# Kernel optimization log

Measured on AMD Instinct MI355X. Metric: run time of the kernel, lower is better.

## Reference

```python
import jax, jax.numpy as jnp
import numpy as np

NUM_ITERS = 10
G_KSIZE, G_SIGMA = 5, 0.5
BIL_KSIZE, BIL_SIG_COLOR, BIL_SIG_SPACE = 5, 0.5, 5.0
EDGE_KSIZE, EDGE_SIG_COLOR, EDGE_SIG_SPACE = 5, 0.5, 5.0


def _gauss1d(ksize, sigma):
    x = jnp.arange(ksize, dtype=jnp.float32) - ksize // 2  # odd ksize -> centered (kornia)
    g = jnp.exp(-(x * x) / (2.0 * sigma * sigma))
    return g / g.sum()


def gaussian_blur(q, ksize, sigma):
    # separable gaussian blur with reflect padding, kornia GaussianBlur2d semantics
    k = _gauss1d(ksize, sigma)
    r = ksize // 2
    B, C, H, W = q.shape
    qp = jnp.pad(q, ((0, 0), (0, 0), (r, r), (0, 0)), mode='reflect')
    q = sum(k[i] * qp[:, :, i:i + H, :] for i in range(ksize))
    qp = jnp.pad(q, ((0, 0), (0, 0), (0, 0), (r, r)), mode='reflect')
    q = sum(k[i] * qp[:, :, :, i:i + W] for i in range(ksize))
    return q


def bilateral_weights(guide, ksize, sigma_color, sigma_space):
    # kornia joint_bilateral_blur weights (l1 color distance, reflect border).
    # guide: [B, Cg, H, W] -> weights [B, K*K, H, W]; guidance is constant across
    # CRF iterations so we precompute the kernel once.
    B, Cg, H, W = guide.shape
    r = ksize // 2
    g1 = _gauss1d(ksize, sigma_space)
    space = jnp.outer(g1, g1)  # normalized 2d gaussian (kornia get_gaussian_kernel2d)
    gp = jnp.pad(guide, ((0, 0), (0, 0), (r, r), (r, r)), mode='reflect')
    inv2sc2 = -0.5 / (sigma_color * sigma_color)
    ws = []
    for dy in range(ksize):
        for dx in range(ksize):
            d = jnp.abs(gp[:, :, dy:dy + H, dx:dx + W] - guide).sum(axis=1)  # [B,H,W]
            ws.append(space[dy, dx] * jnp.exp(inv2sc2 * d * d))
    return jnp.stack(ws, axis=1)  # [B, K*K, H, W]


def bilateral_apply(q, weights, ksize):
    # q: [B,C,H,W], weights: [B,K*K,H,W]
    B, C, H, W = q.shape
    r = ksize // 2
    qp = jnp.pad(q, ((0, 0), (0, 0), (r, r), (r, r)), mode='reflect')
    num = jnp.zeros_like(q)
    idx = 0
    for dy in range(ksize):
        for dx in range(ksize):
            num = num + weights[:, idx][:, None] * qp[:, :, dy:dy + H, dx:dx + W]
            idx += 1
    den = weights.sum(axis=1)[:, None]  # [B,1,H,W]
    return num / den


def _compat(f):
    # compat matrix is -1 off-diagonal, 0 on diagonal:
    # pairwise[c] = -sum_{c'!=c} f[c'] = f[c] - sum_{c'} f[c']
    return f - f.sum(axis=1, keepdims=True)


def setup_inputs() -> dict:
    key = jax.random.key(0)
    k1, k2, k3 = jax.random.split(key, 3)
    B, C, H, W = 2, 21, 512, 512
    unary_logits = jax.random.normal(k1, (B, C, H, W), dtype=jnp.float32)
    image = jax.random.uniform(k2, (B, 3, H, W), dtype=jnp.float32)
    edges = jax.random.uniform(k3, (B, H, W), dtype=jnp.float32)
    return {"unary_logits": unary_logits, "image": image, "edges": edges}


def reference(unary_logits, image, edges):
    edges4 = edges[:, None]  # [B,1,H,W]
    w_rgb = bilateral_weights(image, BIL_KSIZE, BIL_SIG_COLOR, BIL_SIG_SPACE)
    w_edge = bilateral_weights(edges4, EDGE_KSIZE, EDGE_SIG_COLOR, EDGE_SIG_SPACE)
    q = jax.nn.softmax(unary_logits, axis=1)
    for _ in range(NUM_ITERS):
        sf = gaussian_blur(q, G_KSIZE, G_SIGMA)
        rf = bilateral_apply(q, w_rgb, BIL_KSIZE)
        ef = bilateral_apply(q, w_edge, EDGE_KSIZE)
        pairwise = _compat(sf) + _compat(rf) + _compat(ef)
        q = jax.nn.softmax(unary_logits - pairwise, axis=1)
    return q
```

## Files before the change

kernel.cpp:

```cpp
#include <hip/hip_runtime.h>
#include <math.h>

#define BATCH 2
#define NCH 21
#define CPAD 24
#define HH 512
#define WW 512
#define KS 5
#define RAD 2
#define NTAPS 25
#define NUM_ITERS 10

#define TXW 32
#define TYW 8
#define HXW (TXW + 2*RAD)
#define HYW (TYW + 2*RAD)
#define HPXW (HXW * HYW)

#define TW 32
#define TH 16
#define NTHR 512
#define SX 40
#define SY 24
#define SPX (SX * SY)
#define SCHUNK (SPX * 3)
#define EX 36
#define EY 20
#define EPX (EX * EY)
#define RING (EPX - TW*TH)

typedef _Float16 f16;
typedef _Float16 half8 __attribute__((ext_vector_type(8)));
typedef _Float16 half2v __attribute__((ext_vector_type(2)));

__device__ __forceinline__ int refl(int i, int n) {
    if (i < 0) i = -i;
    if (i >= n) i = 2*n - 2 - i;
    return i;
}

#define WSEL(h0, h1, h2, hl, t) \
    ((t) < 8 ? (h0)[(t)] : (t) < 16 ? (h1)[(t) - 8] : (t) < 24 ? (h2)[(t) - 16] : (hl))

__global__ __launch_bounds__(256) void weights_kernel(const float* __restrict__ image,
                                                      const float* __restrict__ edges,
                                                      f16* __restrict__ wcA,
                                                      f16* __restrict__ wcB16) {
    __shared__ float sr_[HYW][HXW];
    __shared__ float sg_[HYW][HXW];
    __shared__ float sb_[HYW][HXW];
    __shared__ float se_[HYW][HXW];

    const int tx = threadIdx.x;
    const int ty = threadIdx.y;
    const int tid = ty * TXW + tx;
    const int x0 = blockIdx.x * TXW;
    const int y0 = blockIdx.y * TYW;
    const int b = blockIdx.z;
    const int x = x0 + tx;
    const int y = y0 + ty;
    const size_t plane = (size_t)HH * WW;
    const float* img = image + (size_t)b * 3 * plane;
    const float* edg = edges + (size_t)b * plane;

    for (int i = tid; i < HPXW; i += TXW * TYW) {
        int ly = i / HXW, lx = i - ly * HXW;
        int gy = refl(y0 + ly - RAD, HH);
        int gx = refl(x0 + lx - RAD, WW);
        int g = gy * WW + gx;
        sr_[ly][lx] = img[g];
        sg_[ly][lx] = img[plane + g];
        sb_[ly][lx] = img[2 * plane + g];
        se_[ly][lx] = edg[g];
    }
    __syncthreads();

    float gs[3];
    gs[0] = 1.0f; gs[1] = __expf(-1.0f / 50.0f); gs[2] = __expf(-4.0f / 50.0f);
    float gb[3];
    gb[0] = 1.0f; gb[1] = __expf(-2.0f); gb[2] = __expf(-8.0f);
    float gbs = gb[0] + 2.0f * (gb[1] + gb[2]);
    gb[0] /= gbs; gb[1] /= gbs; gb[2] /= gbs;

    const float r0 = sr_[ty + RAD][tx + RAD];
    const float g0 = sg_[ty + RAD][tx + RAD];
    const float b0 = sb_[ty + RAD][tx + RAD];
    const float e0 = se_[ty + RAD][tx + RAD];

    float wr[NTAPS], we[NTAPS];
    float sr = 0.f, se = 0.f;
#pragma unroll
    for (int dy = 0; dy < KS; dy++) {
#pragma unroll
        for (int dx = 0; dx < KS; dx++) {
            float sp = gs[abs(dy - RAD)] * gs[abs(dx - RAD)];
            float d = fabsf(sr_[ty + dy][tx + dx] - r0)
                    + fabsf(sg_[ty + dy][tx + dx] - g0)
                    + fabsf(sb_[ty + dy][tx + dx] - b0);
            float w1 = sp * __expf(-2.0f * d * d);
            float de = fabsf(se_[ty + dy][tx + dx] - e0);
            float w2 = sp * __expf(-2.0f * de * de);
            wr[dy * KS + dx] = w1;
            we[dy * KS + dx] = w2;
            sr += w1;
            se += w2;
        }
    }
    float isr = 1.0f / sr, ise = 1.0f / se;
    float wt[NTAPS];
#pragma unroll
    for (int t = 0; t < NTAPS; t++) {
        int dy = t / KS, dx = t % KS;
        float g2 = gb[abs(dy - RAD)] * gb[abs(dx - RAD)];
        wt[t] = g2 + wr[t] * isr + we[t] * ise;
    }
    const size_t pixoff = (size_t)b * plane + (size_t)y * WW + x;
    half8* wo = (half8*)(wcA + pixoff * 24);
#pragma unroll
    for (int g = 0; g < 3; g++) {
        half8 v;
#pragma unroll
        for (int k = 0; k < 8; k++) v[k] = (f16)wt[g * 8 + k];
        wo[g] = v;
    }
    wcB16[pixoff] = (f16)wt[24];
}

__global__ void init_kernel(const float* __restrict__ unary,
                            f16* __restrict__ q,
                            f16* __restrict__ u16) {
    int idx = blockIdx.x * blockDim.x + threadIdx.x;
    if (idx >= BATCH * HH * WW) return;
    int p = idx % (HH * WW);
    int b = idx / (HH * WW);
    const size_t plane = (size_t)HH * WW;
    const float* u = unary + (size_t)b * NCH * plane + p;
    float l[CPAD];
    float m = -1e30f;
#pragma unroll
    for (int c = 0; c < NCH; c++) { l[c] = u[c * plane]; m = fmaxf(m, l[c]); }
    l[21] = 0.f; l[22] = 0.f; l[23] = 0.f;

    half8* uo = (half8*)(u16 + ((size_t)b * plane + p) * CPAD);
#pragma unroll
    for (int g = 0; g < 3; g++) {
        half8 v;
#pragma unroll
        for (int k = 0; k < 8; k++) v[k] = (f16)l[g * 8 + k];
        uo[g] = v;
    }

    float s = 0.f;
    float e[CPAD];
#pragma unroll
    for (int c = 0; c < NCH; c++) { e[c] = __expf(l[c] - m); s += e[c]; }
    float is = 1.0f / s;
    e[21] = 0.f; e[22] = 0.f; e[23] = 0.f;
    half8* qo = (half8*)(q + ((size_t)b * plane + p) * CPAD);
#pragma unroll
    for (int g = 0; g < 3; g++) {
        half8 v;
#pragma unroll
        for (int k = 0; k < 8; k++) v[k] = (f16)(e[g * 8 + k] * is);
        qo[g] = v;
    }
}

#define CONV_ACC_PK(acc2, lds, row0, col0, stride, W0, W1, W2, WL)                     \
    {                                                                                  \
        _Pragma("unroll")                                                              \
        for (int dy = 0; dy < KS; dy++) {                                              \
            _Pragma("unroll")                                                          \
            for (int dx = 0; dx < KS; dx++) {                                          \
                const f16 wt_ = WSEL(W0, W1, W2, WL, dy * KS + dx);                    \
                const half2v wv_ = {wt_, wt_};                                         \
                const f16* tp = (lds) + ((size_t)((row0) + dy) * (stride) + (col0) + dx) * CPAD; \
                half8 v0 = *(const half8*)(tp);                                        \
                half8 v1 = *(const half8*)(tp + 8);                                    \
                half8 v2 = *(const half8*)(tp + 16);                                   \
                acc2[0]  = __builtin_elementwise_fma(wv_, __builtin_shufflevector(v0, v0, 0, 1), acc2[0]);  \
                acc2[1]  = __builtin_elementwise_fma(wv_, __builtin_shufflevector(v0, v0, 2, 3), acc2[1]);  \
                acc2[2]  = __builtin_elementwise_fma(wv_, __builtin_shufflevector(v0, v0, 4, 5), acc2[2]);  \
                acc2[3]  = __builtin_elementwise_fma(wv_, __builtin_shufflevector(v0, v0, 6, 7), acc2[3]);  \
                acc2[4]  = __builtin_elementwise_fma(wv_, __builtin_shufflevector(v1, v1, 0, 1), acc2[4]);  \
                acc2[5]  = __builtin_elementwise_fma(wv_, __builtin_shufflevector(v1, v1, 2, 3), acc2[5]);  \
                acc2[6]  = __builtin_elementwise_fma(wv_, __builtin_shufflevector(v1, v1, 4, 5), acc2[6]);  \
                acc2[7]  = __builtin_elementwise_fma(wv_, __builtin_shufflevector(v1, v1, 6, 7), acc2[7]);  \
                acc2[8]  = __builtin_elementwise_fma(wv_, __builtin_shufflevector(v2, v2, 0, 1), acc2[8]);  \
                acc2[9]  = __builtin_elementwise_fma(wv_, __builtin_shufflevector(v2, v2, 2, 3), acc2[9]);  \
                acc2[10] = __builtin_elementwise_fma(wv_, __builtin_shufflevector(v2, v2, 4, 5), acc2[10]); \
            }                                                                          \
        }                                                                              \
    }

#define LOGITS_FROM_PK(l, acc2, U0, U1, U2)                                            \
    {                                                                                  \
        _Pragma("unroll")                                                              \
        for (int j = 0; j < 10; j++) {                                                 \
            l[2 * j]     = -(float)acc2[j][0];                                         \
            l[2 * j + 1] = -(float)acc2[j][1];                                         \
        }                                                                              \
        l[20] = -(float)acc2[10][0];                                                   \
        _Pragma("unroll")                                                              \
        for (int k = 0; k < 8; k++) l[k] += (float)U0[k];                              \
        _Pragma("unroll")                                                              \
        for (int k = 0; k < 8; k++) l[8 + k] += (float)U1[k];                          \
        _Pragma("unroll")                                                              \
        for (int k = 0; k < 5; k++) l[16 + k] += (float)U2[k];                         \
    }

template <bool FINAL>
__global__ __launch_bounds__(NTHR, 4) void crf_pair_kernel(const f16* __restrict__ qin,
                                                           const f16* __restrict__ u16,
                                                           const f16* __restrict__ wcA,
                                                           const f16* __restrict__ wcB16,
                                                           void* __restrict__ qout) {
    __shared__ __align__(16) f16 buf[SPX][CPAD];

    const int tid = threadIdx.x;
    const int ix = tid & (TW - 1);
    const int iy = tid >> 5;

    const int flat = blockIdx.x;
    const int band = flat & 7;
    const int within = flat >> 3;
    const int b = within >> 6;
    const int r = within & 63;
    const int x0 = (r & 15) * TW;
    const int y0 = (band * 4 + (r >> 4)) * TH;
    const int gx = x0 + ix;
    const int gy = y0 + iy;
    const size_t plane = (size_t)HH * WW;

    const f16* qbase = qin + (size_t)b * plane * CPAD;
    f16* lbase = &buf[0][0];
    for (int idx = tid; idx < SCHUNK; idx += NTHR) {
        int px = idx / 3, h4 = idx - px * 3;
        int sly = px / SX, slx = px - sly * SX;
        int qy = refl(y0 - 4 + sly, HH);
        int qx = refl(x0 - 4 + slx, WW);
        const f16* g = qbase + ((size_t)(qy * WW + qx)) * CPAD + h4 * 8;
        __builtin_amdgcn_global_load_lds(
            (const __attribute__((address_space(1))) void*)g,
            (__attribute__((address_space(3))) void*)(lbase + (size_t)idx * 8),
            16, 0, 0);
    }

    const size_t pixoff = (size_t)b * plane + (size_t)gy * WW + gx;
    const half8* wp = (const half8*)(wcA + pixoff * 24);
    half8 wa0 = wp[0], wa1 = wp[1], wa2 = wp[2];
    f16 wl = wcB16[pixoff];
    const half8* up = (const half8*)(u16 + pixoff * CPAD);
    half8 ui0 = up[0], ui1 = up[1], ui2 = up[2];

    const bool has_ring = tid < RING;
    int rly = 0, rlx = 0;
    half8 wr0 = {}, wr1 = {}, wr2 = {}, ur0 = {}, ur1 = {}, ur2 = {};
    f16 wrl = (f16)0.f;
    if (has_ring) {
        int t = tid;
        if (t < 72)       { rly = t / 36;       rlx = t % 36; }
        else if (t < 144) { t -= 72;  rly = 18 + t / 36; rlx = t % 36; }
        else              { t -= 144; rly = 2 + (t >> 2); int c = t & 3; rlx = (c < 2) ? c : (c + 32); }
        int rgy = y0 + rly - 2, rgx = x0 + rlx - 2;
        int cy = min(max(rgy, 0), HH - 1);
        int cx = min(max(rgx, 0), WW - 1);
        size_t rpo = (size_t)b * plane + (size_t)cy * WW + cx;
        const half8* wpr = (const half8*)(wcA + rpo * 24);
        wr0 = wpr[0]; wr1 = wpr[1]; wr2 = wpr[2];
        wrl = wcB16[rpo];
        const half8* upr = (const half8*)(u16 + rpo * CPAD);
        ur0 = upr[0]; ur1 = upr[1]; ur2 = upr[2];
    }

    __syncthreads();

    half8 qr0, qr1, qr2;
    if (has_ring) {
        half2v acc2[11];
#pragma unroll
        for (int j = 0; j < 11; j++) acc2[j] = (half2v){(f16)0.f, (f16)0.f};
        CONV_ACC_PK(acc2, lbase, rly, rlx, SX, wr0, wr1, wr2, wrl);
        float l[NCH];
        LOGITS_FROM_PK(l, acc2, ur0, ur1, ur2);
        float m = l[0];
#pragma unroll
        for (int c = 1; c < NCH; c++) m = fmaxf(m, l[c]);
        float s = 0.f;
#pragma unroll
        for (int c = 0; c < NCH; c++) { l[c] = __expf(l[c] - m); s += l[c]; }
        float is = 1.0f / s;
#pragma unroll
        for (int k = 0; k < 8; k++) qr0[k] = (f16)(l[k] * is);
#pragma unroll
        for (int k = 0; k < 8; k++) qr1[k] = (f16)(l[8 + k] * is);
#pragma unroll
        for (int k = 0; k < 5; k++) qr2[k] = (f16)(l[16 + k] * is);
        qr2[5] = (f16)0.f; qr2[6] = (f16)0.f; qr2[7] = (f16)0.f;
    }

    half8 qi0, qi1, qi2;
    {
        half2v acc2[11];
#pragma unroll
        for (int j = 0; j < 11; j++) acc2[j] = (half2v){(f16)0.f, (f16)0.f};
        CONV_ACC_PK(acc2, lbase, iy + 2, ix + 2, SX, wa0, wa1, wa2, wl);
        float l[NCH];
        LOGITS_FROM_PK(l, acc2, ui0, ui1, ui2);
        float m = l[0];
#pragma unroll
        for (int c = 1; c < NCH; c++) m = fmaxf(m, l[c]);
        float s = 0.f;
#pragma unroll
        for (int c = 0; c < NCH; c++) { l[c] = __expf(l[c] - m); s += l[c]; }
        float is = 1.0f / s;
#pragma unroll
        for (int k = 0; k < 8; k++) qi0[k] = (f16)(l[k] * is);
#pragma unroll
        for (int k = 0; k < 8; k++) qi1[k] = (f16)(l[8 + k] * is);
#pragma unroll
        for (int k = 0; k < 5; k++) qi2[k] = (f16)(l[16 + k] * is);
        qi2[5] = (f16)0.f; qi2[6] = (f16)0.f; qi2[7] = (f16)0.f;
    }

    __syncthreads();

    {
        half8* d = (half8*)(lbase + ((size_t)(iy + 2) * EX + (ix + 2)) * CPAD);
        d[0] = qi0; d[1] = qi1; d[2] = qi2;
        if (has_ring) {
            half8* dr = (half8*)(lbase + ((size_t)rly * EX + rlx) * CPAD);
            dr[0] = qr0; dr[1] = qr1; dr[2] = qr2;
        }
    }

    __syncthreads();

    {
        int ry[KS], rx[KS];
#pragma unroll
        for (int d = 0; d < KS; d++) {
            ry[d] = refl(gy + d - 2, HH) - (y0 - 2);
            rx[d] = refl(gx + d - 2, WW) - (x0 - 2);
        }
        half2v acc2[11];
#pragma unroll
        for (int j = 0; j < 11; j++) acc2[j] = (half2v){(f16)0.f, (f16)0.f};
#pragma unroll
        for (int dy = 0; dy < KS; dy++) {
#pragma unroll
            for (int dx = 0; dx < KS; dx++) {
                const f16 wt_ = WSEL(wa0, wa1, wa2, wl, dy * KS + dx);
                const half2v wv_ = {wt_, wt_};
                const f16* tp = lbase + ((size_t)ry[dy] * EX + rx[dx]) * CPAD;
                half8 v0 = *(const half8*)(tp);
                half8 v1 = *(const half8*)(tp + 8);
                half8 v2 = *(const half8*)(tp + 16);
                acc2[0]  = __builtin_elementwise_fma(wv_, __builtin_shufflevector(v0, v0, 0, 1), acc2[0]);
                acc2[1]  = __builtin_elementwise_fma(wv_, __builtin_shufflevector(v0, v0, 2, 3), acc2[1]);
                acc2[2]  = __builtin_elementwise_fma(wv_, __builtin_shufflevector(v0, v0, 4, 5), acc2[2]);
                acc2[3]  = __builtin_elementwise_fma(wv_, __builtin_shufflevector(v0, v0, 6, 7), acc2[3]);
                acc2[4]  = __builtin_elementwise_fma(wv_, __builtin_shufflevector(v1, v1, 0, 1), acc2[4]);
                acc2[5]  = __builtin_elementwise_fma(wv_, __builtin_shufflevector(v1, v1, 2, 3), acc2[5]);
                acc2[6]  = __builtin_elementwise_fma(wv_, __builtin_shufflevector(v1, v1, 4, 5), acc2[6]);
                acc2[7]  = __builtin_elementwise_fma(wv_, __builtin_shufflevector(v1, v1, 6, 7), acc2[7]);
                acc2[8]  = __builtin_elementwise_fma(wv_, __builtin_shufflevector(v2, v2, 0, 1), acc2[8]);
                acc2[9]  = __builtin_elementwise_fma(wv_, __builtin_shufflevector(v2, v2, 2, 3), acc2[9]);
                acc2[10] = __builtin_elementwise_fma(wv_, __builtin_shufflevector(v2, v2, 4, 5), acc2[10]);
            }
        }
        float l[NCH];
        LOGITS_FROM_PK(l, acc2, ui0, ui1, ui2);
        float m = l[0];
#pragma unroll
        for (int c = 1; c < NCH; c++) m = fmaxf(m, l[c]);
        float s = 0.f;
#pragma unroll
        for (int c = 0; c < NCH; c++) { l[c] = __expf(l[c] - m); s += l[c]; }
        float is = 1.0f / s;

        if (FINAL) {
            float* qo = (float*)qout + (size_t)b * NCH * plane + (size_t)gy * WW + gx;
#pragma unroll
            for (int c = 0; c < NCH; c++) qo[c * plane] = l[c] * is;
        } else {
            half8* qo = (half8*)((f16*)qout + pixoff * CPAD);
            half8 o0, o1, o2;
#pragma unroll
            for (int k = 0; k < 8; k++) o0[k] = (f16)(l[k] * is);
#pragma unroll
            for (int k = 0; k < 8; k++) o1[k] = (f16)(l[8 + k] * is);
#pragma unroll
            for (int k = 0; k < 5; k++) o2[k] = (f16)(l[16 + k] * is);
            o2[5] = (f16)0.f; o2[6] = (f16)0.f; o2[7] = (f16)0.f;
            qo[0] = o0; qo[1] = o1; qo[2] = o2;
        }
    }
}

extern "C" void kernel_launch(void* const* d_in, const int* in_sizes, int n_in,
                              void* d_out, int out_size, void* d_ws, size_t ws_size,
                              hipStream_t stream) {
    const float* unary = (const float*)d_in[0];
    const float* image = (const float*)d_in[1];
    const float* edges = (const float*)d_in[2];
    float* out = (float*)d_out;

    const size_t plane = (size_t)HH * WW;
    char* ws = (char*)d_ws;
    f16* wcA = (f16*)ws;
    char* p1 = ws + sizeof(f16) * BATCH * plane * 24;
    f16* wcB16 = (f16*)p1;
    char* p2 = p1 + sizeof(f16) * BATCH * plane;
    f16* u16 = (f16*)p2;
    char* p3 = p2 + sizeof(f16) * BATCH * plane * CPAD;
    f16* qA = (f16*)p3;
    f16* qB = qA + (size_t)BATCH * plane * CPAD;

    const int npix = BATCH * HH * WW;
    dim3 gridW(WW / TXW, HH / TYW, BATCH);
    dim3 blockW(TXW, TYW, 1);
    weights_kernel<<<gridW, blockW, 0, stream>>>(image, edges, wcA, wcB16);
    init_kernel<<<(npix + 255) / 256, 256, 0, stream>>>(unary, qA, u16);

    const int nblk = (WW / TW) * (HH / TH) * BATCH;
    f16* qa = qA;
    f16* qb = qB;
    const int npairs = NUM_ITERS / 2;
    for (int it = 0; it < npairs - 1; it++) {
        crf_pair_kernel<false><<<nblk, NTHR, 0, stream>>>(qa, u16, wcA, wcB16, (void*)qb);
        f16* t = qa; qa = qb; qb = t;
    }
    crf_pair_kernel<true><<<nblk, NTHR, 0, stream>>>(qa, u16, wcA, wcB16, (void*)out);
}
```

Measured before the change: 287.5 us.

## Compute two vertical pixels per thread and double tile height

The CRF pair kernel tile height doubles from 16 to 32 rows, with the LDS staging region and the recomputed halo ring resized to match. Each thread now computes two vertically adjacent pixels and sweeps six LDS rows instead of two separate five-row windows, so each LDS load feeds both pixels. This shrinks the halo recompute overhead relative to tile area and cuts LDS reads per output. In exchange it roughly doubles accumulator and weight register use and raises LDS per block, which may reduce occupancy or cause spills under the existing launch bounds.

```diff
diff --git a/kernel.cpp b/kernel.cpp
--- a/kernel.cpp
+++ b/kernel.cpp
@@ -18,14 +18,14 @@
 #define HPXW (HXW * HYW)
 
 #define TW 32
-#define TH 16
+#define TH 32
 #define NTHR 512
 #define SX 40
-#define SY 24
+#define SY 40
 #define SPX (SX * SY)
 #define SCHUNK (SPX * 3)
 #define EX 36
-#define EY 20
+#define EY 36
 #define EPX (EX * EY)
 #define RING (EPX - TW*TH)
 
@@ -166,6 +166,21 @@
     }
 }
 
+#define TAP_PK(acc2, v0, v1, v2, wv_)                                                           \
+    {                                                                                           \
+        acc2[0]  = __builtin_elementwise_fma(wv_, __builtin_shufflevector(v0, v0, 0, 1), acc2[0]);  \
+        acc2[1]  = __builtin_elementwise_fma(wv_, __builtin_shufflevector(v0, v0, 2, 3), acc2[1]);  \
+        acc2[2]  = __builtin_elementwise_fma(wv_, __builtin_shufflevector(v0, v0, 4, 5), acc2[2]);  \
+        acc2[3]  = __builtin_elementwise_fma(wv_, __builtin_shufflevector(v0, v0, 6, 7), acc2[3]);  \
+        acc2[4]  = __builtin_elementwise_fma(wv_, __builtin_shufflevector(v1, v1, 0, 1), acc2[4]);  \
+        acc2[5]  = __builtin_elementwise_fma(wv_, __builtin_shufflevector(v1, v1, 2, 3), acc2[5]);  \
+        acc2[6]  = __builtin_elementwise_fma(wv_, __builtin_shufflevector(v1, v1, 4, 5), acc2[6]);  \
+        acc2[7]  = __builtin_elementwise_fma(wv_, __builtin_shufflevector(v1, v1, 6, 7), acc2[7]);  \
+        acc2[8]  = __builtin_elementwise_fma(wv_, __builtin_shufflevector(v2, v2, 0, 1), acc2[8]);  \
+        acc2[9]  = __builtin_elementwise_fma(wv_, __builtin_shufflevector(v2, v2, 2, 3), acc2[9]);  \
+        acc2[10] = __builtin_elementwise_fma(wv_, __builtin_shufflevector(v2, v2, 4, 5), acc2[10]); \
+    }
+
 #define CONV_ACC_PK(acc2, lds, row0, col0, stride, W0, W1, W2, WL)                     \
     {                                                                                  \
         _Pragma("unroll")                                                              \
@@ -178,17 +193,7 @@
                 half8 v0 = *(const half8*)(tp);                                        \
                 half8 v1 = *(const half8*)(tp + 8);                                    \
                 half8 v2 = *(const half8*)(tp + 16);                                   \
-                acc2[0]  = __builtin_elementwise_fma(wv_, __builtin_shufflevector(v0, v0, 0, 1), acc2[0]);  \
-                acc2[1]  = __builtin_elementwise_fma(wv_, __builtin_shufflevector(v0, v0, 2, 3), acc2[1]);  \
-                acc2[2]  = __builtin_elementwise_fma(wv_, __builtin_shufflevector(v0, v0, 4, 5), acc2[2]);  \
-                acc2[3]  = __builtin_elementwise_fma(wv_, __builtin_shufflevector(v0, v0, 6, 7), acc2[3]);  \
-                acc2[4]  = __builtin_elementwise_fma(wv_, __builtin_shufflevector(v1, v1, 0, 1), acc2[4]);  \
-                acc2[5]  = __builtin_elementwise_fma(wv_, __builtin_shufflevector(v1, v1, 2, 3), acc2[5]);  \
-                acc2[6]  = __builtin_elementwise_fma(wv_, __builtin_shufflevector(v1, v1, 4, 5), acc2[6]);  \
-                acc2[7]  = __builtin_elementwise_fma(wv_, __builtin_shufflevector(v1, v1, 6, 7), acc2[7]);  \
-                acc2[8]  = __builtin_elementwise_fma(wv_, __builtin_shufflevector(v2, v2, 0, 1), acc2[8]);  \
-                acc2[9]  = __builtin_elementwise_fma(wv_, __builtin_shufflevector(v2, v2, 2, 3), acc2[9]);  \
-                acc2[10] = __builtin_elementwise_fma(wv_, __builtin_shufflevector(v2, v2, 4, 5), acc2[10]); \
+                TAP_PK(acc2, v0, v1, v2, wv_);                                         \
             }                                                                          \
         }                                                                              \
     }
@@ -207,6 +212,24 @@
         for (int k = 0; k < 8; k++) l[8 + k] += (float)U1[k];                          \
         _Pragma("unroll")                                                              \
         for (int k = 0; k < 5; k++) l[16 + k] += (float)U2[k];                         \
+    }
+
+#define SOFTMAX_PACK(l, O0, O1, O2)                                                    \
+    {                                                                                  \
+        float m = l[0];                                                                \
+        _Pragma("unroll")                                                              \
+        for (int c = 1; c < NCH; c++) m = fmaxf(m, l[c]);                              \
+        float s = 0.f;                                                                 \
+        _Pragma("unroll")                                                              \
+        for (int c = 0; c < NCH; c++) { l[c] = __expf(l[c] - m); s += l[c]; }          \
+        float is = 1.0f / s;                                                           \
+        _Pragma("unroll")                                                              \
+        for (int k = 0; k < 8; k++) O0[k] = (f16)(l[k] * is);                          \
+        _Pragma("unroll")                                                              \
+        for (int k = 0; k < 8; k++) O1[k] = (f16)(l[8 + k] * is);                      \
+        _Pragma("unroll")                                                              \
+        for (int k = 0; k < 5; k++) O2[k] = (f16)(l[16 + k] * is);                     \
+        O2[5] = (f16)0.f; O2[6] = (f16)0.f; O2[7] = (f16)0.f;                          \
     }
 
 template <bool FINAL>
@@ -218,18 +241,18 @@
     __shared__ __align__(16) f16 buf[SPX][CPAD];
 
     const int tid = threadIdx.x;
-    const int ix = tid & (TW - 1);
-    const int iy = tid >> 5;
+    const int ixv = tid & (TW - 1);
+    const int iyv = tid >> 5;
 
     const int flat = blockIdx.x;
     const int band = flat & 7;
     const int within = flat >> 3;
-    const int b = within >> 6;
-    const int r = within & 63;
+    const int b = within >> 5;
+    const int r = within & 31;
     const int x0 = (r & 15) * TW;
-    const int y0 = (band * 4 + (r >> 4)) * TH;
-    const int gx = x0 + ix;
-    const int gy = y0 + iy;
+    const int y0 = (band * 2 + (r >> 4)) * TH;
+    const int gx = x0 + ixv;
+    const int gy0 = y0 + 2 * iyv;
     const size_t plane = (size_t)HH * WW;
 
     const f16* qbase = qin + (size_t)b * plane * CPAD;
@@ -246,12 +269,18 @@
             16, 0, 0);
     }
 
-    const size_t pixoff = (size_t)b * plane + (size_t)gy * WW + gx;
-    const half8* wp = (const half8*)(wcA + pixoff * 24);
-    half8 wa0 = wp[0], wa1 = wp[1], wa2 = wp[2];
-    f16 wl = wcB16[pixoff];
-    const half8* up = (const half8*)(u16 + pixoff * CPAD);
-    half8 ui0 = up[0], ui1 = up[1], ui2 = up[2];
+    const size_t pixoff0 = (size_t)b * plane + (size_t)gy0 * WW + gx;
+    const size_t pixoff1 = pixoff0 + WW;
+    const half8* wp0 = (const half8*)(wcA + pixoff0 * 24);
+    half8 wa0 = wp0[0], wa1 = wp0[1], wa2 = wp0[2];
+    f16 wl0 = wcB16[pixoff0];
+    const half8* wp1 = (const half8*)(wcA + pixoff1 * 24);
+    half8 wb0 = wp1[0], wb1 = wp1[1], wb2 = wp1[2];
+    f16 wl1 = wcB16[pixoff1];
+    const half8* up0 = (const half8*)(u16 + pixoff0 * CPAD);
+    half8 uA0 = up0[0], uA1 = up0[1], uA2 = up0[2];
+    const half8* up1 = (const half8*)(u16 + pixoff1 * CPAD);
+    half8 uB0 = up1[0], uB1 = up1[1], uB2 = up1[2];
 
     const bool has_ring = tid < RING;
     int rly = 0, rlx = 0;
@@ -259,9 +288,8 @@
     f16 wrl = (f16)0.f;
     if (has_ring) {
         int t = tid;
-        if (t < 72)       { rly = t / 36;       rlx = t % 36; }
-        else if (t < 144) { t -= 72;  rly = 18 + t / 36; rlx = t % 36; }
-        else              { t -= 144; rly = 2 + (t >> 2); int c = t & 3; rlx = (c < 2) ? c : (c + 32); }
+        if (t < 144) { int rr = t / 36; rly = (rr < 2) ? rr : 32 + rr; rlx = t % 36; }
+        else         { int t2 = t - 144; rly = 2 + (t2 >> 2); int c = t2 & 3; rlx = (c < 2) ? c : (c + 32); }
         int rgy = y0 + rly - 2, rgx = x0 + rlx - 2;
         int cy = min(max(rgy, 0), HH - 1);
         int cx = min(max(rgx, 0), WW - 1);
@@ -283,51 +311,53 @@
         CONV_ACC_PK(acc2, lbase, rly, rlx, SX, wr0, wr1, wr2, wrl);
         float l[NCH];
         LOGITS_FROM_PK(l, acc2, ur0, ur1, ur2);
-        float m = l[0];
-#pragma unroll
-        for (int c = 1; c < NCH; c++) m = fmaxf(m, l[c]);
-        float s = 0.f;
-#pragma unroll
-        for (int c = 0; c < NCH; c++) { l[c] = __expf(l[c] - m); s += l[c]; }
-        float is = 1.0f / s;
-#pragma unroll
-        for (int k = 0; k < 8; k++) qr0[k] = (f16)(l[k] * is);
-#pragma unroll
-        for (int k = 0; k < 8; k++) qr1[k] = (f16)(l[8 + k] * is);
-#pragma unroll
-        for (int k = 0; k < 5; k++) qr2[k] = (f16)(l[16 + k] * is);
-        qr2[5] = (f16)0.f; qr2[6] = (f16)0.f; qr2[7] = (f16)0.f;
-    }
-
-    half8 qi0, qi1, qi2;
+        SOFTMAX_PACK(l, qr0, qr1, qr2);
+    }
+
+    half8 qiA0, qiA1, qiA2, qiB0, qiB1, qiB2;
     {
-        half2v acc2[11];
-#pragma unroll
-        for (int j = 0; j < 11; j++) acc2[j] = (half2v){(f16)0.f, (f16)0.f};
-        CONV_ACC_PK(acc2, lbase, iy + 2, ix + 2, SX, wa0, wa1, wa2, wl);
+        half2v accA[11], accB[11];
+#pragma unroll
+        for (int j = 0; j < 11; j++) {
+            accA[j] = (half2v){(f16)0.f, (f16)0.f};
+            accB[j] = (half2v){(f16)0.f, (f16)0.f};
+        }
+        const int row0 = 2 * iyv + 2;
+        const int col0 = ixv + 2;
+#pragma unroll
+        for (int dy = 0; dy < 6; dy++) {
+#pragma unroll
+            for (int dx = 0; dx < KS; dx++) {
+                const f16* tp = lbase + ((size_t)(row0 + dy) * SX + col0 + dx) * CPAD;
+                half8 v0 = *(const half8*)(tp);
+                half8 v1 = *(const half8*)(tp + 8);
+                half8 v2 = *(const half8*)(tp + 16);
+                if (dy < 5) {
+                    const f16 wt_ = WSEL(wa0, wa1, wa2, wl0, dy * KS + dx);
+                    const half2v wv_ = {wt_, wt_};
+                    TAP_PK(accA, v0, v1, v2, wv_);
+                }
+                if (dy >= 1) {
+                    const f16 wt_ = WSEL(wb0, wb1, wb2, wl1, (dy - 1) * KS + dx);
+                    const half2v wv_ = {wt_, wt_};
+                    TAP_PK(accB, v0, v1, v2, wv_);
+                }
+            }
+        }
         float l[NCH];
-        LOGITS_FROM_PK(l, acc2, ui0, ui1, ui2);
-        float m = l[0];
-#pragma unroll
-        for (int c = 1; c < NCH; c++) m = fmaxf(m, l[c]);
-        float s = 0.f;
-#pragma unroll
-        for (int c = 0; c < NCH; c++) { l[c] = __expf(l[c] - m); s += l[c]; }
-        float is = 1.0f / s;
-#pragma unroll
-        for (int k = 0; k < 8; k++) qi0[k] = (f16)(l[k] * is);
-#pragma unroll
-        for (int k = 0; k < 8; k++) qi1[k] = (f16)(l[8 + k] * is);
-#pragma unroll
-        for (int k = 0; k < 5; k++) qi2[k] = (f16)(l[16 + k] * is);
-        qi2[5] = (f16)0.f; qi2[6] = (f16)0.f; qi2[7] = (f16)0.f;
+        LOGITS_FROM_PK(l, accA, uA0, uA1, uA2);
+        SOFTMAX_PACK(l, qiA0, qiA1, qiA2);
+        LOGITS_FROM_PK(l, accB, uB0, uB1, uB2);
+        SOFTMAX_PACK(l, qiB0, qiB1, qiB2);
     }
 
     __syncthreads();
 
     {
-        half8* d = (half8*)(lbase + ((size_t)(iy + 2) * EX + (ix + 2)) * CPAD);
-        d[0] = qi0; d[1] = qi1; d[2] = qi2;
+        half8* d0 = (half8*)(lbase + ((size_t)(2 * iyv + 2) * EX + (ixv + 2)) * CPAD);
+        d0[0] = qiA0; d0[1] = qiA1; d0[2] = qiA2;
+        half8* d1 = (half8*)(lbase + ((size_t)(2 * iyv + 3) * EX + (ixv + 2)) * CPAD);
+        d1[0] = qiB0; d1[1] = qiB1; d1[2] = qiB2;
         if (has_ring) {
             half8* dr = (half8*)(lbase + ((size_t)rly * EX + rlx) * CPAD);
             dr[0] = qr0; dr[1] = qr1; dr[2] = qr2;
@@ -337,63 +367,67 @@
     __syncthreads();
 
     {
-        int ry[KS], rx[KS];
-#pragma unroll
-        for (int d = 0; d < KS; d++) {
-            ry[d] = refl(gy + d - 2, HH) - (y0 - 2);
-            rx[d] = refl(gx + d - 2, WW) - (x0 - 2);
-        }
-        half2v acc2[11];
-#pragma unroll
-        for (int j = 0; j < 11; j++) acc2[j] = (half2v){(f16)0.f, (f16)0.f};
-#pragma unroll
-        for (int dy = 0; dy < KS; dy++) {
+        int ryy[6], rxx[KS];
+#pragma unroll
+        for (int d = 0; d < 6; d++) ryy[d] = refl(gy0 + d - 2, HH) - (y0 - 2);
+#pragma unroll
+        for (int d = 0; d < KS; d++) rxx[d] = refl(gx + d - 2, WW) - (x0 - 2);
+
+        half2v accA[11], accB[11];
+#pragma unroll
+        for (int j = 0; j < 11; j++) {
+            accA[j] = (half2v){(f16)0.f, (f16)0.f};
+            accB[j] = (half2v){(f16)0.f, (f16)0.f};
+        }
+#pragma unroll
+        for (int dy = 0; dy < 6; dy++) {
 #pragma unroll
             for (int dx = 0; dx < KS; dx++) {
-                const f16 wt_ = WSEL(wa0, wa1, wa2, wl, dy * KS + dx);
-                const half2v wv_ = {wt_, wt_};
-                const f16* tp = lbase + ((size_t)ry[dy] * EX + rx[dx]) * CPAD;
+                const f16* tp = lbase + ((size_t)ryy[dy] * EX + rxx[dx]) * CPAD;
                 half8 v0 = *(const half8*)(tp);
                 half8 v1 = *(const half8*)(tp + 8);
                 half8 v2 = *(const half8*)(tp + 16);
-                acc2[0]  = __builtin_elementwise_fma(wv_, __builtin_shufflevector(v0, v0, 0, 1), acc2[0]);
-                acc2[1]  = __builtin_elementwise_fma(wv_, __builtin_shufflevector(v0, v0, 2, 3), acc2[1]);
-                acc2[2]  = __builtin_elementwise_fma(wv_, __builtin_shufflevector(v0, v0, 4, 5), acc2[2]);
-                acc2[3]  = __builtin_elementwise_fma(wv_, __builtin_shufflevector(v0, v0, 6, 7), acc2[3]);
-                acc2[4]  = __builtin_elementwise_fma(wv_, __builtin_shufflevector(v1, v1, 0, 1), acc2[4]);
-                acc2[5]  = __builtin_elementwise_fma(wv_, __builtin_shufflevector(v1, v1, 2, 3), acc2[5]);
-                acc2[6]  = __builtin_elementwise_fma(wv_, __builtin_shufflevector(v1, v1, 4, 5), acc2[6]);
-                acc2[7]  = __builtin_elementwise_fma(wv_, __builtin_shufflevector(v1, v1, 6, 7), acc2[7]);
-                acc2[8]  = __builtin_elementwise_fma(wv_, __builtin_shufflevector(v2, v2, 0, 1), acc2[8]);
-                acc2[9]  = __builtin_elementwise_fma(wv_, __builtin_shufflevector(v2, v2, 2, 3), acc2[9]);
-                acc2[10] = __builtin_elementwise_fma(wv_, __builtin_shufflevector(v2, v2, 4, 5), acc2[10]);
+                if (dy < 5) {
+                    const f16 wt_ = WSEL(wa0, wa1, wa2, wl0, dy * KS + dx);
+                    const half2v wv_ = {wt_, wt_};
+                    TAP_PK(accA, v0, v1, v2, wv_);
+                }
+                if (dy >= 1) {
+                    const f16 wt_ = WSEL(wb0, wb1, wb2, wl1, (dy - 1) * KS + dx);
+                    const half2v wv_ = {wt_, wt_};
+                    TAP_PK(accB, v0, v1, v2, wv_);
+                }
             }
         }
-        float l[NCH];
-        LOGITS_FROM_PK(l, acc2, ui0, ui1, ui2);
-        float m = l[0];
-#pragma unroll
-        for (int c = 1; c < NCH; c++) m = fmaxf(m, l[c]);
-        float s = 0.f;
-#pragma unroll
-        for (int c = 0; c < NCH; c++) { l[c] = __expf(l[c] - m); s += l[c]; }
-        float is = 1.0f / s;
+        float l0[NCH], l1[NCH];
+        LOGITS_FROM_PK(l0, accA, uA0, uA1, uA2);
+        LOGITS_FROM_PK(l1, accB, uB0, uB1, uB2);
 
         if (FINAL) {
-            float* qo = (float*)qout + (size_t)b * NCH * plane + (size_t)gy * WW + gx;
-#pragma unroll
-            for (int c = 0; c < NCH; c++) qo[c * plane] = l[c] * is;
+            float m0 = l0[0], m1 = l1[0];
+#pragma unroll
+            for (int c = 1; c < NCH; c++) { m0 = fmaxf(m0, l0[c]); m1 = fmaxf(m1, l1[c]); }
+            float s0 = 0.f, s1 = 0.f;
+#pragma unroll
+            for (int c = 0; c < NCH; c++) {
+                l0[c] = __expf(l0[c] - m0); s0 += l0[c];
+                l1[c] = __expf(l1[c] - m1); s1 += l1[c];
+            }
+            float is0 = 1.0f / s0, is1 = 1.0f / s1;
+            float* qo = (float*)qout + (size_t)b * NCH * plane + (size_t)gy0 * WW + gx;
+#pragma unroll
+            for (int c = 0; c < NCH; c++) {
+                qo[c * plane] = l0[c] * is0;
+                qo[c * plane + WW] = l1[c] * is1;
+            }
         } else {
-            half8* qo = (half8*)((f16*)qout + pixoff * CPAD);
             half8 o0, o1, o2;
-#pragma unroll
-            for (int k = 0; k < 8; k++) o0[k] = (f16)(l[k] * is);
-#pragma unroll
-            for (int k = 0; k < 8; k++) o1[k] = (f16)(l[8 + k] * is);
-#pragma unroll
-            for (int k = 0; k < 5; k++) o2[k] = (f16)(l[16 + k] * is);
-            o2[5] = (f16)0.f; o2[6] = (f16)0.f; o2[7] = (f16)0.f;
-            qo[0] = o0; qo[1] = o1; qo[2] = o2;
+            SOFTMAX_PACK(l0, o0, o1, o2);
+            half8* q0 = (half8*)((f16*)qout + pixoff0 * CPAD);
+            q0[0] = o0; q0[1] = o1; q0[2] = o2;
+            SOFTMAX_PACK(l1, o0, o1, o2);
+            half8* q1 = (half8*)((f16*)qout + pixoff1 * CPAD);
+            q1[0] = o0; q1[1] = o1; q1[2] = o2;
         }
     }
 }
```

After: 831.7 us. +189.3%, slower.
